# Kernel tuning notes

Hardware: AMD Instinct MI355X
Metric: run time of the kernel (lower is better)

## Reference

```python
import jax, jax.numpy as jnp
import numpy as np

N, IN_DIM, H, L, NH, LAT = 4096, 16, 128, 4, 8, 16
HD = H // NH
FF = 2 * H
DR_THR = 0.2
LN_EPS = 1e-5


def _ln(x, s, b):
    m = x.mean(-1, keepdims=True)
    v = ((x - m) ** 2).mean(-1, keepdims=True)
    return (x - m) * jax.lax.rsqrt(v + LN_EPS) * s + b


def compute_dr_mask(x_raw):
    eta = x_raw[:, 1] * (2.62 - (-2.62)) + (-2.62)
    phi = x_raw[:, 2] * (3.1416 - (-3.1416)) + (-3.1416)
    deta = eta[:, None] - eta[None, :]
    dphi = phi[:, None] - phi[None, :]
    dphi = jnp.arctan2(jnp.sin(dphi), jnp.cos(dphi))
    dr = jnp.sqrt(deta ** 2 + dphi ** 2)
    return jnp.where(dr <= DR_THR, 0.0, -jnp.inf).astype(jnp.float32)


def setup_inputs() -> dict:
    key = jax.random.key(0)
    ks = jax.random.split(key, 32)
    g = lambda i, shape, s=0.02: (jax.random.normal(ks[i], shape, dtype=jnp.float32) * s)
    inp = {
        'x_raw': jax.random.uniform(ks[0], (N, IN_DIM), dtype=jnp.float32),
        'batch': jnp.zeros((N,), dtype=jnp.int64) if jax.config.read('jax_enable_x64') else jnp.zeros((N,), dtype=jnp.int32),
        'in_w': g(1, (H, IN_DIM), 0.1), 'in_b': jnp.zeros((H,), jnp.float32),
        'ln1_s': jnp.ones((L, H), jnp.float32), 'ln1_b': jnp.zeros((L, H), jnp.float32),
        'qkv_w': g(2, (L, 3 * H, H)), 'qkv_b': jnp.zeros((L, 3 * H), jnp.float32),
        'ao_w': g(3, (L, H, H)), 'ao_b': jnp.zeros((L, H), jnp.float32),
        'ln2_s': jnp.ones((L, H), jnp.float32), 'ln2_b': jnp.zeros((L, H), jnp.float32),
        'f1_w': g(4, (L, FF, H)), 'f1_b': jnp.zeros((L, FF), jnp.float32),
        'f2_w': g(5, (L, H, FF)), 'f2_b': jnp.zeros((L, H), jnp.float32),
        'lat1_w': g(6, (H, H), 0.08), 'lat1_b': jnp.zeros((H,), jnp.float32),
        'lat2_w': g(7, (LAT, H), 0.08), 'lat2_b': jnp.zeros((LAT,), jnp.float32),
        'b1_w': g(8, (H // 2, H), 0.08), 'b1_b': jnp.zeros((H // 2,), jnp.float32),
        'b2_w': g(9, (1, H // 2), 0.008), 'b2_b': jnp.full((1,), -3.0, jnp.float32),
    }
    return inp


def reference(x_raw, batch, in_w, in_b, ln1_s, ln1_b, qkv_w, qkv_b, ao_w, ao_b,
              ln2_s, ln2_b, f1_w, f1_b, f2_w, f2_b,
              lat1_w, lat1_b, lat2_w, lat2_b, b1_w, b1_b, b2_w, b2_b):
    mask = jax.lax.stop_gradient(compute_dr_mask(x_raw))  # [N, N] additive mask
    x = x_raw @ in_w.T + in_b  # [N, H]
    scale = 1.0 / jnp.sqrt(jnp.float32(HD))
    for l in range(L):  # norm_first TransformerEncoderLayer, eval mode (no dropout)
        h = _ln(x, ln1_s[l], ln1_b[l])
        qkv = h @ qkv_w[l].T + qkv_b[l]
        q, k, v = [t.reshape(N, NH, HD) for t in jnp.split(qkv, 3, axis=-1)]
        scores = jnp.einsum('qhd,khd->hqk', q, k) * scale + mask[None]
        attn = jax.nn.softmax(scores, axis=-1)
        o = jnp.einsum('hqk,khd->qhd', attn, v).reshape(N, H)
        x = x + o @ ao_w[l].T + ao_b[l]
        h2 = _ln(x, ln2_s[l], ln2_b[l])
        x = x + jax.nn.relu(h2 @ f1_w[l].T + f1_b[l]) @ f2_w[l].T + f2_b[l]
    lat = jax.nn.relu(x @ lat1_w.T + lat1_b) @ lat2_w.T + lat2_b  # [N, LAT]
    lat = lat / jnp.maximum(jnp.linalg.norm(lat, axis=-1, keepdims=True), 1e-12)
    beta = jax.nn.sigmoid(jax.nn.relu(x @ b1_w.T + b1_b) @ b2_w.T + b2_b)
    beta = jnp.clip(beta, 1e-6, 1 - 1e-6)  # [N, 1]
    return beta, lat
```

## Files before the change

kernel.cpp:

```cpp
#include <hip/hip_runtime.h>
#include <hip/hip_bf16.h>

typedef unsigned short u16;
typedef short short8_t __attribute__((ext_vector_type(8)));
typedef float floatx4 __attribute__((ext_vector_type(4)));

constexpr int NT = 4096, H = 128, CAP = 64;
constexpr int GRID = 256, BLK = 512, GSTRIDE = GRID * BLK;
constexpr int NGRP = 8, GRPSZ = GRID / NGRP;

constexpr int OFF_QKV  = 0;
constexpr int OFF_AO   = 196608;
constexpr int OFF_F1   = 262144;
constexpr int OFF_F2   = 393216;
constexpr int OFF_LAT1 = 524288;
constexpr int OFF_B1   = 540672;
constexpr int OFF_LAT2 = 548864;
constexpr int W_TOTAL  = 550912;

__device__ __forceinline__ float bfu(u16 u) { return __uint_as_float(((unsigned)u) << 16); }
__device__ __forceinline__ u16 f2bf(float f) {
  unsigned u = __float_as_uint(f);
  u += 0x7fffu + ((u >> 16) & 1u);
  return (u16)(u >> 16);
}
__device__ __forceinline__ void unpack8(uint4 u, float* f) {
  f[0] = __uint_as_float(u.x << 16); f[1] = __uint_as_float(u.x & 0xffff0000u);
  f[2] = __uint_as_float(u.y << 16); f[3] = __uint_as_float(u.y & 0xffff0000u);
  f[4] = __uint_as_float(u.z << 16); f[5] = __uint_as_float(u.z & 0xffff0000u);
  f[6] = __uint_as_float(u.w << 16); f[7] = __uint_as_float(u.w & 0xffff0000u);
}
__device__ __forceinline__ short8_t cvt8(const float* bp) {
  const float4 f0 = *(const float4*)bp, f1 = *(const float4*)(bp + 4);
  short8_t r;
  r[0] = (short)f2bf(f0.x); r[1] = (short)f2bf(f0.y);
  r[2] = (short)f2bf(f0.z); r[3] = (short)f2bf(f0.w);
  r[4] = (short)f2bf(f1.x); r[5] = (short)f2bf(f1.y);
  r[6] = (short)f2bf(f1.z); r[7] = (short)f2bf(f1.w);
  return r;
}

__device__ __forceinline__ void st64(unsigned long long* p, unsigned long long v) {
  __hip_atomic_store(p, v, __ATOMIC_RELAXED, __HIP_MEMORY_SCOPE_AGENT);
}
__device__ __forceinline__ void st16(u16* p, u16 v) {
  __hip_atomic_store(p, v, __ATOMIC_RELAXED, __HIP_MEMORY_SCOPE_AGENT);
}

__device__ __forceinline__ void gridbar(int* bar, int grp, int e) {
  __syncthreads();
  if (threadIdx.x == 0) {
    asm volatile("" ::: "memory");
    int* root = bar;
    int* gcnt = bar + 16 + 16 * grp;
    const int old = __hip_atomic_fetch_add(gcnt, 1, __ATOMIC_RELAXED,
                                           __HIP_MEMORY_SCOPE_AGENT);
    if (old == GRPSZ * e - 1)
      __hip_atomic_fetch_add(root, 1, __ATOMIC_RELAXED, __HIP_MEMORY_SCOPE_AGENT);
    while (__hip_atomic_load(root, __ATOMIC_RELAXED, __HIP_MEMORY_SCOPE_AGENT) < NGRP * e)
      __builtin_amdgcn_s_sleep(2);
    asm volatile("" ::: "memory");
  }
  __syncthreads();
}

struct Prm {
  const float *xr, *in_w, *in_b, *ln1_s, *ln1_b, *qkv_w, *qkv_b, *ao_w, *ao_b,
              *ln2_s, *ln2_b, *f1_w, *f1_b, *f2_w, *f2_b, *lat1_w, *lat1_b,
              *lat2_w, *lat2_b, *b1_w, *b1_b, *b2_w, *b2_b;
  u16* W; u16* KV[4]; int* bar; float* out;
};

__global__ __launch_bounds__(BLK, 2) void fused_kernel(Prm p) {
  const int t = threadIdx.x, bid = blockIdx.x;
  const int lane = t & 63, w = t >> 6;
  const int lr = lane & 15, quad = lane >> 4;
  const int gtid = bid * BLK + t;
  const int r0 = bid * 16;
  const int grp = bid >> 5;
  const floatx4 FZ = {0.f, 0.f, 0.f, 0.f};
  int bar_k = 0;

  const int pr = t >> 2, sub = t & 3;
  const int lq = pr >> 3, h = pr & 7;
  float qv[16];

  __shared__ float Xs[16][132];
  __shared__ int NIs[16][CAP];
  __shared__ int NCs[16];
  __shared__ union {
    unsigned long long words[8][64];
    struct { u16 A16[16][152]; u16 FF1[16][280]; } g;
    u16 QS[16][384];
  } sm;

  auto stage_x = [&](const float* sc, const float* bi, bool do_ln) {
    const int r = t >> 5, j0 = (t & 31) * 4;
    const float4 xv = *(const float4*)&Xs[r][j0];
    float v0 = xv.x, v1 = xv.y, v2 = xv.z, v3 = xv.w;
    if (do_ln) {
      float s = v0 + v1 + v2 + v3;
      float ss = v0 * v0 + v1 * v1 + v2 * v2 + v3 * v3;
#pragma unroll
      for (int off = 1; off <= 16; off <<= 1) {
        s += __shfl_xor(s, off); ss += __shfl_xor(ss, off);
      }
      const float mean = s * (1.f / 128.f);
      const float rstd = rsqrtf(ss * (1.f / 128.f) - mean * mean + 1e-5f);
      v0 = (v0 - mean) * rstd * sc[j0]     + bi[j0];
      v1 = (v1 - mean) * rstd * sc[j0 + 1] + bi[j0 + 1];
      v2 = (v2 - mean) * rstd * sc[j0 + 2] + bi[j0 + 2];
      v3 = (v3 - mean) * rstd * sc[j0 + 3] + bi[j0 + 3];
    }
    uint2 pk;
    pk.x = (unsigned)f2bf(v0) | ((unsigned)f2bf(v1) << 16);
    pk.y = (unsigned)f2bf(v2) | ((unsigned)f2bf(v3) << 16);
    *(uint2*)&sm.g.A16[r][j0] = pk;
  };

  auto load_qv = [&]() {
    const u16* qp = &sm.QS[lq][h * 16];
    uint4 a = *(const uint4*)qp, b = *(const uint4*)(qp + 8);
    unpack8(a, qv); unpack8(b, qv + 8);
#pragma unroll
    for (int d = 0; d < 16; ++d) qv[d] *= 0.25f;
  };

  for (int i = 49152 + gtid; i < W_TOTAL; i += GSTRIDE) {
    float v;
    if      (i < OFF_AO)   v = p.qkv_w[i];
    else if (i < OFF_F1)   v = p.ao_w[i - OFF_AO];
    else if (i < OFF_F2)   v = p.f1_w[i - OFF_F1];
    else if (i < OFF_LAT1) v = p.f2_w[i - OFF_F2];
    else if (i < OFF_B1)   v = p.lat1_w[i - OFF_LAT1];
    else if (i < OFF_LAT2) v = p.b1_w[i - OFF_B1];
    else                   v = p.lat2_w[i - OFF_LAT2];
    st16(&p.W[i], f2bf(v));
  }
  for (int i = t; i < 16 * H; i += BLK) {
    const int r = i >> 7, c = i & 127;
    const float* xp = p.xr + (size_t)(r0 + r) * 16;
    const float* wp = p.in_w + c * 16;
    float acc = p.in_b[c];
#pragma unroll
    for (int k = 0; k < 16; ++k) acc += xp[k] * wp[k];
    Xs[r][c] = acc;
  }
  for (int uu = 0; uu < 2; ++uu) {
    const int q0 = r0 + uu * 8;
    double qe[8], qp_[8];
#pragma unroll
    for (int j = 0; j < 8; ++j) {
      qe[j]  = (double)p.xr[(q0 + j) * 16 + 1] * 5.24 - 2.62;
      qp_[j] = (double)p.xr[(q0 + j) * 16 + 2] * 6.2832 - 3.1416;
    }
    for (int c = 0; c < 8; ++c) {
      const int k = c * 512 + t;
      const double ke = (double)p.xr[k * 16 + 1] * 5.24 - 2.62;
      const double kp = (double)p.xr[k * 16 + 2] * 6.2832 - 3.1416;
#pragma unroll
      for (int j = 0; j < 8; ++j) {
        const double de = qe[j] - ke;
        double dp = qp_[j] - kp;
        dp -= 6.283185307179586 * rint(dp * 0.15915494309189535);
        const unsigned long long bm = __ballot((de * de + dp * dp) <= 0.04);
        if (lane == 0) sm.words[j][c * 8 + w] = bm;
      }
    }
    __syncthreads();
    {
      unsigned long long m = sm.words[w][lane];
      const int cnt = __popcll(m);
      int incl = cnt;
#pragma unroll
      for (int off = 1; off < 64; off <<= 1) {
        const int n = __shfl_up(incl, off);
        if (lane >= off) incl += n;
      }
      int pos = incl - cnt;
      const int lq2 = uu * 8 + w;
      const int kbase = (lane >> 3) * 512 + (lane & 7) * 64;
      while (m) {
        const int b = __builtin_ctzll(m);
        m &= m - 1;
        if (pos < CAP) NIs[lq2][pos] = kbase + b;
        ++pos;
      }
      if (lane == 63) NCs[lq2] = incl > CAP ? CAP : incl;
    }
    __syncthreads();
  }
  stage_x(p.ln1_s, p.ln1_b, true);
  __syncthreads();
  {
    const int c0 = w * 48;
    floatx4 a0 = FZ, a1 = FZ, a2 = FZ;
#pragma unroll
    for (int k0 = 0; k0 < 128; k0 += 32) {
      short8_t a  = *(const short8_t*)&sm.g.A16[lr][k0 + quad * 8];
      short8_t b0 = cvt8(&p.qkv_w[(size_t)(c0 + lr) * 128 + k0 + quad * 8]);
      short8_t b1 = cvt8(&p.qkv_w[(size_t)(c0 + 16 + lr) * 128 + k0 + quad * 8]);
      short8_t b2 = cvt8(&p.qkv_w[(size_t)(c0 + 32 + lr) * 128 + k0 + quad * 8]);
      a0 = __builtin_amdgcn_mfma_f32_16x16x32_bf16(a, b0, a0, 0, 0, 0);
      a1 = __builtin_amdgcn_mfma_f32_16x16x32_bf16(a, b1, a1, 0, 0, 0);
      a2 = __builtin_amdgcn_mfma_f32_16x16x32_bf16(a, b2, a2, 0, 0, 0);
    }
    __syncthreads();
#pragma unroll
    for (int r = 0; r < 4; ++r) {
      const int row = quad * 4 + r;
      sm.QS[row][c0 + lr]      = f2bf(a0[r] + p.qkv_b[c0 + lr]);
      sm.QS[row][c0 + 16 + lr] = f2bf(a1[r] + p.qkv_b[c0 + 16 + lr]);
      sm.QS[row][c0 + 32 + lr] = f2bf(a2[r] + p.qkv_b[c0 + 32 + lr]);
    }
    __syncthreads();
    load_qv();
    unsigned long long* d64 = (unsigned long long*)(p.KV[0] + (size_t)r0 * 256);
    for (int j = t; j < 16 * 64; j += BLK) {
      const int row = j >> 6;
      st64(&d64[j], ((const unsigned long long*)&sm.QS[row][128])[j & 63]);
    }
  }
  gridbar(p.bar, grp, ++bar_k);

  for (int l = 0; l < 4; ++l) {
    const u16* __restrict__ kvsrc = p.KV[l];
    u16* __restrict__ kvdst = (l < 3) ? p.KV[l + 1] : nullptr;

    {
      float o[16];
#pragma unroll
      for (int d = 0; d < 16; ++d) o[d] = 0.f;
      float se = 0.f;
      const int cnt = NCs[lq];
      int i = sub;
      uint4 ck0, ck1, cv0, cv1;
      if (i < cnt) {
        const u16* kp = kvsrc + (size_t)NIs[lq][i] * 256 + h * 16;
        ck0 = *(const uint4*)kp;         ck1 = *(const uint4*)(kp + 8);
        cv0 = *(const uint4*)(kp + 128); cv1 = *(const uint4*)(kp + 136);
      }
      while (i < cnt) {
        const int inx = i + 4;
        uint4 nk0, nk1, nv0, nv1;
        if (inx < cnt) {
          const u16* kp = kvsrc + (size_t)NIs[lq][inx] * 256 + h * 16;
          nk0 = *(const uint4*)kp;         nk1 = *(const uint4*)(kp + 8);
          nv0 = *(const uint4*)(kp + 128); nv1 = *(const uint4*)(kp + 136);
        }
        float kv[16], vv[16];
        unpack8(ck0, kv); unpack8(ck1, kv + 8);
        unpack8(cv0, vv); unpack8(cv1, vv + 8);
        float s0 = 0.f, s1 = 0.f, s2 = 0.f, s3 = 0.f;
#pragma unroll
        for (int d = 0; d < 16; d += 4) {
          s0 += qv[d] * kv[d];         s1 += qv[d + 1] * kv[d + 1];
          s2 += qv[d + 2] * kv[d + 2]; s3 += qv[d + 3] * kv[d + 3];
        }
        const float e = __expf((s0 + s1) + (s2 + s3));
        se += e;
#pragma unroll
        for (int d = 0; d < 16; ++d) o[d] += e * vv[d];
        ck0 = nk0; ck1 = nk1; cv0 = nv0; cv1 = nv1;
        i = inx;
      }
#pragma unroll
      for (int d = 0; d < 16; ++d) o[d] += __shfl_xor(o[d], 1);
      se += __shfl_xor(se, 1);
#pragma unroll
      for (int d = 0; d < 16; ++d) o[d] += __shfl_xor(o[d], 2);
      se += __shfl_xor(se, 2);
      if (sub == 0) {
        const float inv = 1.f / se;
        uint4 w0, w1;
        w0.x = (unsigned)f2bf(o[0] * inv)  | ((unsigned)f2bf(o[1] * inv) << 16);
        w0.y = (unsigned)f2bf(o[2] * inv)  | ((unsigned)f2bf(o[3] * inv) << 16);
        w0.z = (unsigned)f2bf(o[4] * inv)  | ((unsigned)f2bf(o[5] * inv) << 16);
        w0.w = (unsigned)f2bf(o[6] * inv)  | ((unsigned)f2bf(o[7] * inv) << 16);
        w1.x = (unsigned)f2bf(o[8] * inv)  | ((unsigned)f2bf(o[9] * inv) << 16);
        w1.y = (unsigned)f2bf(o[10] * inv) | ((unsigned)f2bf(o[11] * inv) << 16);
        w1.z = (unsigned)f2bf(o[12] * inv) | ((unsigned)f2bf(o[13] * inv) << 16);
        w1.w = (unsigned)f2bf(o[14] * inv) | ((unsigned)f2bf(o[15] * inv) << 16);
        *(uint4*)&sm.g.A16[lq][h * 16]     = w0;
        *(uint4*)&sm.g.A16[lq][h * 16 + 8] = w1;
      }
    }
    __syncthreads();
    {
      const u16* Bw = p.W + OFF_AO + l * 16384;
      const float* ab = p.ao_b + l * 128;
      const int col = w * 16 + lr;
      floatx4 acc = FZ;
#pragma unroll
      for (int k0 = 0; k0 < 128; k0 += 32) {
        short8_t a = *(const short8_t*)&sm.g.A16[lr][k0 + quad * 8];
        short8_t b = *(const short8_t*)&Bw[(size_t)col * 128 + k0 + quad * 8];
        acc = __builtin_amdgcn_mfma_f32_16x16x32_bf16(a, b, acc, 0, 0, 0);
      }
      const float bv = ab[col];
#pragma unroll
      for (int r = 0; r < 4; ++r)
        Xs[quad * 4 + r][col] += acc[r] + bv;
    }
    __syncthreads();
    stage_x(p.ln2_s + l * 128, p.ln2_b + l * 128, true);
    __syncthreads();
    {
      const u16* Bw = p.W + OFF_F1 + l * 32768;
      const float* fb = p.f1_b + l * 256;
      const int c0 = w * 32;
      floatx4 a0 = FZ, a1 = FZ;
#pragma unroll
      for (int k0 = 0; k0 < 128; k0 += 32) {
        short8_t a  = *(const short8_t*)&sm.g.A16[lr][k0 + quad * 8];
        short8_t b0 = *(const short8_t*)&Bw[(size_t)(c0 + lr) * 128 + k0 + quad * 8];
        short8_t b1 = *(const short8_t*)&Bw[(size_t)(c0 + 16 + lr) * 128 + k0 + quad * 8];
        a0 = __builtin_amdgcn_mfma_f32_16x16x32_bf16(a, b0, a0, 0, 0, 0);
        a1 = __builtin_amdgcn_mfma_f32_16x16x32_bf16(a, b1, a1, 0, 0, 0);
      }
#pragma unroll
      for (int r = 0; r < 4; ++r) {
        const int row = quad * 4 + r;
        sm.g.FF1[row][c0 + lr]      = f2bf(fmaxf(a0[r] + fb[c0 + lr], 0.f));
        sm.g.FF1[row][c0 + 16 + lr] = f2bf(fmaxf(a1[r] + fb[c0 + 16 + lr], 0.f));
      }
    }
    __syncthreads();
    {
      const u16* Bw = p.W + OFF_F2 + l * 32768;
      const float* fb = p.f2_b + l * 128;
      const int col = w * 16 + lr;
      floatx4 acc = FZ;
#pragma unroll
      for (int k0 = 0; k0 < 256; k0 += 32) {
        short8_t a = *(const short8_t*)&sm.g.FF1[lr][k0 + quad * 8];
        short8_t b = *(const short8_t*)&Bw[(size_t)col * 256 + k0 + quad * 8];
        acc = __builtin_amdgcn_mfma_f32_16x16x32_bf16(a, b, acc, 0, 0, 0);
      }
      const float bv = fb[col];
#pragma unroll
      for (int r = 0; r < 4; ++r)
        Xs[quad * 4 + r][col] += acc[r] + bv;
    }
    __syncthreads();
    if (l < 3) {
      stage_x(p.ln1_s + (l + 1) * 128, p.ln1_b + (l + 1) * 128, true);
      __syncthreads();
      {
        const u16* Bw = p.W + OFF_QKV + (l + 1) * 49152;
        const float* qb = p.qkv_b + (l + 1) * 384;
        const int c0 = w * 48;
        floatx4 a0 = FZ, a1 = FZ, a2 = FZ;
#pragma unroll
        for (int k0 = 0; k0 < 128; k0 += 32) {
          short8_t a  = *(const short8_t*)&sm.g.A16[lr][k0 + quad * 8];
          short8_t b0 = *(const short8_t*)&Bw[(size_t)(c0 + lr) * 128 + k0 + quad * 8];
          short8_t b1 = *(const short8_t*)&Bw[(size_t)(c0 + 16 + lr) * 128 + k0 + quad * 8];
          short8_t b2 = *(const short8_t*)&Bw[(size_t)(c0 + 32 + lr) * 128 + k0 + quad * 8];
          a0 = __builtin_amdgcn_mfma_f32_16x16x32_bf16(a, b0, a0, 0, 0, 0);
          a1 = __builtin_amdgcn_mfma_f32_16x16x32_bf16(a, b1, a1, 0, 0, 0);
          a2 = __builtin_amdgcn_mfma_f32_16x16x32_bf16(a, b2, a2, 0, 0, 0);
        }
        __syncthreads();
#pragma unroll
        for (int r = 0; r < 4; ++r) {
          const int row = quad * 4 + r;
          sm.QS[row][c0 + lr]      = f2bf(a0[r] + qb[c0 + lr]);
          sm.QS[row][c0 + 16 + lr] = f2bf(a1[r] + qb[c0 + 16 + lr]);
          sm.QS[row][c0 + 32 + lr] = f2bf(a2[r] + qb[c0 + 32 + lr]);
        }
        __syncthreads();
        load_qv();
        unsigned long long* d64 = (unsigned long long*)(kvdst + (size_t)r0 * 256);
        for (int j = t; j < 16 * 64; j += BLK) {
          const int row = j >> 6;
          st64(&d64[j], ((const unsigned long long*)&sm.QS[row][128])[j & 63]);
        }
      }
      gridbar(p.bar, grp, ++bar_k);
    } else {
      stage_x(nullptr, nullptr, false);
      __syncthreads();
      {
        const int c0 = w * 32;
        if (c0 < 192) {
          const u16* Bw = p.W + OFF_LAT1;
          floatx4 a0 = FZ, a1 = FZ;
#pragma unroll
          for (int k0 = 0; k0 < 128; k0 += 32) {
            short8_t a  = *(const short8_t*)&sm.g.A16[lr][k0 + quad * 8];
            short8_t b0 = *(const short8_t*)&Bw[(size_t)(c0 + lr) * 128 + k0 + quad * 8];
            short8_t b1 = *(const short8_t*)&Bw[(size_t)(c0 + 16 + lr) * 128 + k0 + quad * 8];
            a0 = __builtin_amdgcn_mfma_f32_16x16x32_bf16(a, b0, a0, 0, 0, 0);
            a1 = __builtin_amdgcn_mfma_f32_16x16x32_bf16(a, b1, a1, 0, 0, 0);
          }
          const int cA = c0 + lr, cB = c0 + 16 + lr;
          const float bA = cA < 128 ? p.lat1_b[cA] : p.b1_b[cA - 128];
          const float bB = cB < 128 ? p.lat1_b[cB] : p.b1_b[cB - 128];
#pragma unroll
          for (int r = 0; r < 4; ++r) {
            const int row = quad * 4 + r;
            sm.g.FF1[row][cA] = f2bf(fmaxf(a0[r] + bA, 0.f));
            sm.g.FF1[row][cB] = f2bf(fmaxf(a1[r] + bB, 0.f));
          }
        }
      }
      __syncthreads();
      if (t < 256) {
        const int r = t >> 4, c = t & 15;
        float acc = p.lat2_b[c];
        const u16* gw = p.W + OFF_LAT2 + c * 128;
        for (int k = 0; k < 128; ++k) acc += bfu(sm.g.FF1[r][k]) * bfu(gw[k]);
        float ss = acc * acc;
        ss += __shfl_xor(ss, 1); ss += __shfl_xor(ss, 2);
        ss += __shfl_xor(ss, 4); ss += __shfl_xor(ss, 8);
        p.out[NT + (size_t)(r0 + r) * 16 + c] = acc / fmaxf(sqrtf(ss), 1e-12f);
        float v = 0.f;
#pragma unroll
        for (int i = 0; i < 4; ++i)
          v += bfu(sm.g.FF1[r][128 + c * 4 + i]) * p.b2_w[c * 4 + i];
        v += __shfl_xor(v, 1); v += __shfl_xor(v, 2);
        v += __shfl_xor(v, 4); v += __shfl_xor(v, 8);
        if (c == 0) {
          v += p.b2_b[0];
          const float beta = 1.f / (1.f + __expf(-v));
          p.out[r0 + r] = fminf(fmaxf(beta, 1e-6f), 1.f - 1e-6f);
        }
      }
    }
  }
}

extern "C" void kernel_launch(void* const* d_in, const int* in_sizes, int n_in,
                              void* d_out, int out_size, void* d_ws, size_t ws_size,
                              hipStream_t stream) {
  Prm prm;
  prm.xr    = (const float*)d_in[0];
  prm.in_w  = (const float*)d_in[2];  prm.in_b  = (const float*)d_in[3];
  prm.ln1_s = (const float*)d_in[4];  prm.ln1_b = (const float*)d_in[5];
  prm.qkv_w = (const float*)d_in[6];  prm.qkv_b = (const float*)d_in[7];
  prm.ao_w  = (const float*)d_in[8];  prm.ao_b  = (const float*)d_in[9];
  prm.ln2_s = (const float*)d_in[10]; prm.ln2_b = (const float*)d_in[11];
  prm.f1_w  = (const float*)d_in[12]; prm.f1_b  = (const float*)d_in[13];
  prm.f2_w  = (const float*)d_in[14]; prm.f2_b  = (const float*)d_in[15];
  prm.lat1_w= (const float*)d_in[16]; prm.lat1_b= (const float*)d_in[17];
  prm.lat2_w= (const float*)d_in[18]; prm.lat2_b= (const float*)d_in[19];
  prm.b1_w  = (const float*)d_in[20]; prm.b1_b  = (const float*)d_in[21];
  prm.b2_w  = (const float*)d_in[22]; prm.b2_b  = (const float*)d_in[23];
  prm.out   = (float*)d_out;

  char* pw = (char*)d_ws;
  prm.W    = (u16*)pw;   pw += ((size_t)W_TOTAL * 2 + 255) & ~(size_t)255;
  for (int i = 0; i < 4; ++i) { prm.KV[i] = (u16*)pw; pw += (size_t)NT * 256 * 2; }
  prm.bar  = (int*)pw;   pw += 2048;

  hipMemsetAsync(prm.bar, 0, 2048, stream);
  fused_kernel<<<GRID, BLK, 0, stream>>>(prm);
}
```

Baseline: 193.7 us.

## Spatially bin points by eta/phi and permute rows so blocks hold nearby points

Adds a counting-sort of all points into a 27x32 eta/phi grid, using global atomics and three extra grid barriers, to build a permutation. Each block then processes 16 spatially adjacent points, and block-to-row mapping is interleaved across barrier groups. Outputs are scattered back to the original indices. The intent is that neighbor sets within a block overlap, which should improve locality and balance in the sparse attention gather. The cost is extra barriers and atomics, plus a nondeterministic order within each bin.

```diff
diff --git a/kernel.cpp b/kernel.cpp
--- a/kernel.cpp
+++ b/kernel.cpp
@@ -8,6 +8,7 @@
 constexpr int NT = 4096, H = 128, CAP = 64;
 constexpr int GRID = 256, BLK = 512, GSTRIDE = GRID * BLK;
 constexpr int NGRP = 8, GRPSZ = GRID / NGRP;
+constexpr int NBIN = 27 * 32;
 
 constexpr int OFF_QKV  = 0;
 constexpr int OFF_AO   = 196608;
@@ -46,6 +47,12 @@
 __device__ __forceinline__ void st16(u16* p, u16 v) {
   __hip_atomic_store(p, v, __ATOMIC_RELAXED, __HIP_MEMORY_SCOPE_AGENT);
 }
+__device__ __forceinline__ void st32(int* p, int v) {
+  __hip_atomic_store(p, v, __ATOMIC_RELAXED, __HIP_MEMORY_SCOPE_AGENT);
+}
+__device__ __forceinline__ int aadd(int* p, int v) {
+  return __hip_atomic_fetch_add(p, v, __ATOMIC_RELAXED, __HIP_MEMORY_SCOPE_AGENT);
+}
 
 __device__ __forceinline__ void gridbar(int* bar, int grp, int e) {
   __syncthreads();
@@ -53,10 +60,9 @@
     asm volatile("" ::: "memory");
     int* root = bar;
     int* gcnt = bar + 16 + 16 * grp;
-    const int old = __hip_atomic_fetch_add(gcnt, 1, __ATOMIC_RELAXED,
-                                           __HIP_MEMORY_SCOPE_AGENT);
+    const int old = aadd(gcnt, 1);
     if (old == GRPSZ * e - 1)
-      __hip_atomic_fetch_add(root, 1, __ATOMIC_RELAXED, __HIP_MEMORY_SCOPE_AGENT);
+      aadd(root, 1);
     while (__hip_atomic_load(root, __ATOMIC_RELAXED, __HIP_MEMORY_SCOPE_AGENT) < NGRP * e)
       __builtin_amdgcn_s_sleep(2);
     asm volatile("" ::: "memory");
@@ -68,7 +74,7 @@
   const float *xr, *in_w, *in_b, *ln1_s, *ln1_b, *qkv_w, *qkv_b, *ao_w, *ao_b,
               *ln2_s, *ln2_b, *f1_w, *f1_b, *f2_w, *f2_b, *lat1_w, *lat1_b,
               *lat2_w, *lat2_b, *b1_w, *b1_b, *b2_w, *b2_b;
-  u16* W; u16* KV[4]; int* bar; float* out;
+  u16* W; u16* KV[4]; int* bar; int* bincnt; int* binoff; int* Pm; float* out;
 };
 
 __global__ __launch_bounds__(BLK, 2) void fused_kernel(Prm p) {
@@ -76,7 +82,7 @@
   const int lane = t & 63, w = t >> 6;
   const int lr = lane & 15, quad = lane >> 4;
   const int gtid = bid * BLK + t;
-  const int r0 = bid * 16;
+  const int r0 = ((bid & 7) * 32 + (bid >> 3)) * 16;
   const int grp = bid >> 5;
   const floatx4 FZ = {0.f, 0.f, 0.f, 0.f};
   int bar_k = 0;
@@ -88,11 +94,21 @@
   __shared__ float Xs[16][132];
   __shared__ int NIs[16][CAP];
   __shared__ int NCs[16];
+  __shared__ int Orig[16];
+  __shared__ int wt8[8];
   __shared__ union {
     unsigned long long words[8][64];
     struct { u16 A16[16][152]; u16 FF1[16][280]; } g;
     u16 QS[16][384];
   } sm;
+
+  auto binkey = [&](int orig) {
+    const float eta = p.xr[orig * 16 + 1] * 5.24f - 2.62f;
+    const float phi = p.xr[orig * 16 + 2] * 6.2832f - 3.1416f;
+    int be = (int)((eta + 2.62f) * 5.0f);  be = be < 0 ? 0 : (be > 26 ? 26 : be);
+    int bp = (int)((phi + 3.1416f) * 5.0f); bp = bp < 0 ? 0 : (bp > 31 ? 31 : bp);
+    return be * 32 + bp;
+  };
 
   auto stage_x = [&](const float* sc, const float* bi, bool do_ln) {
     const int r = t >> 5, j0 = (t & 31) * 4;
@@ -126,6 +142,7 @@
     for (int d = 0; d < 16; ++d) qv[d] *= 0.25f;
   };
 
+  if (t < 16) aadd(&p.bincnt[binkey(bid * 16 + t)], 1);
   for (int i = 49152 + gtid; i < W_TOTAL; i += GSTRIDE) {
     float v;
     if      (i < OFF_AO)   v = p.qkv_w[i];
@@ -137,9 +154,39 @@
     else                   v = p.lat2_w[i - OFF_LAT2];
     st16(&p.W[i], f2bf(v));
   }
+  gridbar(p.bar, grp, ++bar_k);
+  if (bid == 0) {
+    const int i0 = t * 2, i1 = t * 2 + 1;
+    const int c0 = (i0 < NBIN) ? p.bincnt[i0] : 0;
+    const int c1 = (i1 < NBIN) ? p.bincnt[i1] : 0;
+    const int s = c0 + c1;
+    int incl = s;
+#pragma unroll
+    for (int off = 1; off < 64; off <<= 1) {
+      const int n = __shfl_up(incl, off);
+      if (lane >= off) incl += n;
+    }
+    if (lane == 63) wt8[w] = incl;
+    __syncthreads();
+    int woff = 0;
+    for (int j = 0; j < w; ++j) woff += wt8[j];
+    const int excl = woff + incl - s;
+    if (i0 < NBIN) st32(&p.binoff[i0], excl);
+    if (i1 < NBIN) st32(&p.binoff[i1], excl + c0);
+  }
+  gridbar(p.bar, grp, ++bar_k);
+  if (t < 16) {
+    const int orig = bid * 16 + t;
+    const int pos = aadd(&p.binoff[binkey(orig)], 1);
+    st32(&p.Pm[pos], orig);
+  }
+  gridbar(p.bar, grp, ++bar_k);
+  if (t < 16) Orig[t] = p.Pm[r0 + t];
+  __syncthreads();
+
   for (int i = t; i < 16 * H; i += BLK) {
     const int r = i >> 7, c = i & 127;
-    const float* xp = p.xr + (size_t)(r0 + r) * 16;
+    const float* xp = p.xr + (size_t)Orig[r] * 16;
     const float* wp = p.in_w + c * 16;
     float acc = p.in_b[c];
 #pragma unroll
@@ -147,17 +194,17 @@
     Xs[r][c] = acc;
   }
   for (int uu = 0; uu < 2; ++uu) {
-    const int q0 = r0 + uu * 8;
     double qe[8], qp_[8];
 #pragma unroll
     for (int j = 0; j < 8; ++j) {
-      qe[j]  = (double)p.xr[(q0 + j) * 16 + 1] * 5.24 - 2.62;
-      qp_[j] = (double)p.xr[(q0 + j) * 16 + 2] * 6.2832 - 3.1416;
+      const int oq = Orig[uu * 8 + j];
+      qe[j]  = (double)p.xr[oq * 16 + 1] * 5.24 - 2.62;
+      qp_[j] = (double)p.xr[oq * 16 + 2] * 6.2832 - 3.1416;
     }
     for (int c = 0; c < 8; ++c) {
-      const int k = c * 512 + t;
-      const double ke = (double)p.xr[k * 16 + 1] * 5.24 - 2.62;
-      const double kp = (double)p.xr[k * 16 + 2] * 6.2832 - 3.1416;
+      const int ok = p.Pm[c * 512 + t];
+      const double ke = (double)p.xr[ok * 16 + 1] * 5.24 - 2.62;
+      const double kp = (double)p.xr[ok * 16 + 2] * 6.2832 - 3.1416;
 #pragma unroll
       for (int j = 0; j < 8; ++j) {
         const double de = qe[j] - ke;
@@ -408,13 +455,14 @@
       __syncthreads();
       if (t < 256) {
         const int r = t >> 4, c = t & 15;
+        const int orig = Orig[r];
         float acc = p.lat2_b[c];
         const u16* gw = p.W + OFF_LAT2 + c * 128;
         for (int k = 0; k < 128; ++k) acc += bfu(sm.g.FF1[r][k]) * bfu(gw[k]);
         float ss = acc * acc;
         ss += __shfl_xor(ss, 1); ss += __shfl_xor(ss, 2);
         ss += __shfl_xor(ss, 4); ss += __shfl_xor(ss, 8);
-        p.out[NT + (size_t)(r0 + r) * 16 + c] = acc / fmaxf(sqrtf(ss), 1e-12f);
+        p.out[NT + (size_t)orig * 16 + c] = acc / fmaxf(sqrtf(ss), 1e-12f);
         float v = 0.f;
 #pragma unroll
         for (int i = 0; i < 4; ++i)
@@ -424,7 +472,7 @@
         if (c == 0) {
           v += p.b2_b[0];
           const float beta = 1.f / (1.f + __expf(-v));
-          p.out[r0 + r] = fminf(fmaxf(beta, 1e-6f), 1.f - 1e-6f);
+          p.out[orig] = fminf(fmaxf(beta, 1e-6f), 1.f - 1e-6f);
         }
       }
     }
@@ -450,10 +498,13 @@
   prm.out   = (float*)d_out;
 
   char* pw = (char*)d_ws;
-  prm.W    = (u16*)pw;   pw += ((size_t)W_TOTAL * 2 + 255) & ~(size_t)255;
+  prm.W      = (u16*)pw; pw += ((size_t)W_TOTAL * 2 + 255) & ~(size_t)255;
   for (int i = 0; i < 4; ++i) { prm.KV[i] = (u16*)pw; pw += (size_t)NT * 256 * 2; }
-  prm.bar  = (int*)pw;   pw += 2048;
-
-  hipMemsetAsync(prm.bar, 0, 2048, stream);
+  prm.bar    = (int*)pw; pw += 2048;
+  prm.bincnt = (int*)pw; pw += 4096;
+  prm.binoff = (int*)pw; pw += 4096;
+  prm.Pm     = (int*)pw; pw += NT * 4;
+
+  hipMemsetAsync(prm.bar, 0, 2048 + 4096, stream);
   fused_kernel<<<GRID, BLK, 0, stream>>>(prm);
 }
```

Result: slower. 223.4 us (+15.4%).
